# Kernel tuning notes

Measured on AMD Instinct MI355X. Metric: run time of the kernel, lower is better.

Reference implementation:

```python
import jax, jax.numpy as jnp
import numpy as np

N_NODES = 100000
N_EDGES = 6400000


def setup_inputs() -> dict:
    key = jax.random.key(0)
    k_x, k_e, k_w1, k_w2 = jax.random.split(key, 4)
    x = jax.random.normal(k_x, (N_NODES, 1), dtype=jnp.float32)
    edge_index = jax.random.randint(k_e, (2, N_EDGES), 0, N_NODES, dtype=jnp.int64)
    # Glorot-ish init for the tiny GCN linears
    W1 = jax.random.normal(k_w1, (1, 16), dtype=jnp.float32) * (1.0 / np.sqrt(1))
    b1 = jnp.zeros((16,), dtype=jnp.float32)
    W2 = jax.random.normal(k_w2, (16, 1), dtype=jnp.float32) * (1.0 / np.sqrt(16))
    b2 = jnp.zeros((1,), dtype=jnp.float32)
    return {"x": x, "edge_index": edge_index, "W1": W1, "b1": b1, "W2": W2, "b2": b2}


def _gcn_forward(x, row, col, norm, W1, b1, W2, b2, n):
    def conv(h, W, b):
        h = h @ W                                   # [N, d_out] linear first (PyG GCNConv)
        msg = h[row] * norm[:, None]                # gather + symmetric norm
        out = jax.ops.segment_sum(msg, col, num_segments=n)  # scatter-add to targets
        return out + b

    h = jax.nn.relu(conv(x, W1, b1))
    return conv(h, W2, b2)


def reference(x, edge_index, W1, b1, W2, b2):
    n = x.shape[0]
    # add self loops (GCNConv default add_self_loops=True)
    loop = jnp.arange(n, dtype=edge_index.dtype)
    row = jnp.concatenate([edge_index[0], loop])    # source j
    col = jnp.concatenate([edge_index[1], loop])    # target i
    # symmetric normalization D^{-1/2} (A+I) D^{-1/2}
    deg = jax.ops.segment_sum(jnp.ones_like(row, dtype=x.dtype), col, num_segments=n)
    deg_inv_sqrt = jnp.where(deg > 0, jax.lax.rsqrt(jnp.maximum(deg, 1.0)), 0.0)
    norm = deg_inv_sqrt[row] * deg_inv_sqrt[col]    # [E+N]
    return _gcn_forward(x, row, col, norm, W1, b1, W2, b2, n)
```

## Files before the change

kernel.cpp:

```cpp
#include <hip/hip_runtime.h>

#define BLK    256
#define NH     1024
#define SCAN_T 1024
#define SHIFT  13
#define CHUNK  8192
#define BPB    64
#define MAXNB  32



__global__ void k_hist(const int* __restrict__ col, int* __restrict__ hist,
                       int E, int NB) {
    __shared__ int h[MAXNB];
    for (int j = threadIdx.x; j < NB; j += BLK) h[j] = 0;
    __syncthreads();
    int stride = gridDim.x * blockDim.x;
    for (int e = blockIdx.x * blockDim.x + threadIdx.x; e < E; e += stride)
        atomicAdd(&h[col[e] >> SHIFT], 1);
    __syncthreads();
    for (int j = threadIdx.x; j < NB; j += BLK)
        hist[blockIdx.x * NB + j] = h[j];
}

__global__ void k_colscan(const int* __restrict__ hist, int* __restrict__ colOff,
                          int* __restrict__ totals, int NB) {
    __shared__ int lds[SCAN_T];
    int p = blockIdx.x, t = threadIdx.x;
    int v = hist[t * NB + p];
    lds[t] = v;
    __syncthreads();
    for (int off = 1; off < SCAN_T; off <<= 1) {
        int add = (t >= off) ? lds[t - off] : 0;
        __syncthreads();
        lds[t] += add;
        __syncthreads();
    }
    colOff[t * NB + p] = lds[t] - v;
    if (t == SCAN_T - 1) totals[p] = lds[t];
}

__global__ void k_binscan(const int* __restrict__ totals, int* __restrict__ binstart,
                          int NB) {
    if (blockIdx.x == 0 && threadIdx.x == 0) {
        int run = 0;
        for (int p = 0; p < NB; ++p) { binstart[p] = run; run += totals[p]; }
        binstart[NB] = run;
    }
}

__global__ void k_scatter(const int* __restrict__ row, const int* __restrict__ col,
                          const int* __restrict__ colOff, const int* __restrict__ binstart,
                          int* __restrict__ rows, int* __restrict__ colsl,
                          int E, int NB) {
    __shared__ int cur[MAXNB];
    for (int j = threadIdx.x; j < NB; j += BLK)
        cur[j] = binstart[j] + colOff[blockIdx.x * NB + j];
    __syncthreads();
    int stride = gridDim.x * blockDim.x;
    for (int e = blockIdx.x * blockDim.x + threadIdx.x; e < E; e += stride) {
        int c = col[e];
        int p = c >> SHIFT;
        int pos = atomicAdd(&cur[p], 1);
        rows[pos]  = row[e];
        colsl[pos] = c & (CHUNK - 1);
    }
}

template <bool GATHER>
__global__ void k_bagg(const int* __restrict__ rows, const int* __restrict__ colsl,
                       const int* __restrict__ binstart, const float* __restrict__ src,
                       float* __restrict__ partial) {
    __shared__ float acc[CHUNK];
    int p = blockIdx.x / BPB, q = blockIdx.x % BPB;
    for (int j = threadIdx.x; j < CHUNK; j += BLK) acc[j] = 0.0f;
    __syncthreads();
    int s = binstart[p], t = binstart[p + 1];
    long long len = t - s;
    int lo = s + (int)(len * q / BPB);
    int hi = s + (int)(len * (q + 1) / BPB);
    for (int e = lo + threadIdx.x; e < hi; e += BLK) {
        float v = GATHER ? src[rows[e]] : 1.0f;
        atomicAdd(&acc[colsl[e]], v);
    }
    __syncthreads();
    float* out = partial + (size_t)blockIdx.x * CHUNK;
    for (int j = threadIdx.x; j < CHUNK; j += BLK) out[j] = acc[j];
}

__device__ __forceinline__ float red_sum(const float* __restrict__ partial, int i) {
    int p = i >> SHIFT, il = i & (CHUNK - 1);
    const float* base = partial + ((size_t)p * BPB) * CHUNK + il;
    float s = 0.0f;
#pragma unroll
    for (int q = 0; q < BPB; ++q) s += base[(size_t)q * CHUNK];
    return s;
}

__global__ void k_red_deg_node1(const float* __restrict__ partial, const float* __restrict__ x,
                                float* __restrict__ dis, float* __restrict__ xs,
                                float* __restrict__ tself, int n) {
    int i = blockIdx.x * blockDim.x + threadIdx.x;
    if (i >= n) return;
    float d = rsqrtf(red_sum(partial, i) + 1.0f);
    dis[i] = d;
    float v = x[i] * d;
    xs[i] = v;
    tself[i] = v;
}

__global__ void k_red_node2(const float* __restrict__ partial, const float* __restrict__ dis,
                            float* __restrict__ t_gs, float* __restrict__ u,
                            const float* __restrict__ W1, const float* __restrict__ b1,
                            const float* __restrict__ W2, int n) {
    int i = blockIdx.x * blockDim.x + threadIdx.x;
    if (i >= n) return;
    float tt = t_gs[i] + red_sum(partial, i);
    float a = dis[i] * tt;
    float g = 0.0f;
#pragma unroll
    for (int k = 0; k < 16; ++k) {
        float h = fmaf(a, W1[k], b1[k]);
        h = fmaxf(h, 0.0f);
        g = fmaf(h, W2[k], g);
    }
    float v = g * dis[i];
    t_gs[i] = v;
    u[i]    = v;
}

__global__ void k_red_out(const float* __restrict__ partial, const float* __restrict__ dis,
                          float* __restrict__ u_out, const float* __restrict__ b2, int n) {
    int i = blockIdx.x * blockDim.x + threadIdx.x;
    if (i >= n) return;
    float uu = u_out[i] + red_sum(partial, i);
    u_out[i] = fmaf(dis[i], uu, b2[0]);
}


__global__ void k_zero(int* __restrict__ p, int n) {
    int i = blockIdx.x * blockDim.x + threadIdx.x;
    if (i < n) p[i] = 0;
}
__global__ void k_deg(const int* __restrict__ col, int* __restrict__ deg, int E) {
    int stride = gridDim.x * blockDim.x;
    for (int e = blockIdx.x * blockDim.x + threadIdx.x; e < E; e += stride)
        atomicAdd(&deg[col[e]], 1);
}
__global__ void k_agg(const int* __restrict__ row, const int* __restrict__ col,
                      const float* __restrict__ src, float* __restrict__ dst, int E) {
    int stride = gridDim.x * blockDim.x;
    for (int e = blockIdx.x * blockDim.x + threadIdx.x; e < E; e += stride)
        unsafeAtomicAdd(&dst[col[e]], src[row[e]]);
}
__global__ void k_node1(const float* __restrict__ x, int* __restrict__ deg_i,
                        float* __restrict__ xs, float* __restrict__ t, int n) {
    int i = blockIdx.x * blockDim.x + threadIdx.x;
    if (i < n) {
        float d = rsqrtf((float)deg_i[i] + 1.0f);
        reinterpret_cast<float*>(deg_i)[i] = d;
        float v = x[i] * d;
        xs[i] = v;
        t[i]  = v;
    }
}
__global__ void k_node2(const float* __restrict__ dis, float* __restrict__ t_gs,
                        const float* __restrict__ W1, const float* __restrict__ b1,
                        const float* __restrict__ W2, float* __restrict__ u, int n) {
    int i = blockIdx.x * blockDim.x + threadIdx.x;
    if (i < n) {
        float a = dis[i] * t_gs[i];
        float g = 0.0f;
#pragma unroll
        for (int k = 0; k < 16; ++k) {
            float h = fmaf(a, W1[k], b1[k]);
            h = fmaxf(h, 0.0f);
            g = fmaf(h, W2[k], g);
        }
        float v = g * dis[i];
        t_gs[i] = v;
        u[i]    = v;
    }
}
__global__ void k_out(const float* __restrict__ dis, float* __restrict__ u_out,
                      const float* __restrict__ b2, int n) {
    int i = blockIdx.x * blockDim.x + threadIdx.x;
    if (i < n) u_out[i] = fmaf(dis[i], u_out[i], b2[0]);
}


extern "C" void kernel_launch(void* const* d_in, const int* in_sizes, int n_in,
                              void* d_out, int out_size, void* d_ws, size_t ws_size,
                              hipStream_t stream) {
    const float* x   = (const float*)d_in[0];
    const int*   idx = (const int*)d_in[1];
    const float* W1  = (const float*)d_in[2];
    const float* b1  = (const float*)d_in[3];
    const float* W2  = (const float*)d_in[4];
    const float* b2  = (const float*)d_in[5];

    int n = in_sizes[0];
    int E = in_sizes[1] / 2;
    const int* row = idx;
    const int* col = idx + E;

    int NB = (n + CHUNK - 1) >> SHIFT;

    float* wsf = (float*)d_ws;
    size_t o = 0;
    float* dis      = wsf + o;            o += (size_t)n;
    float* ws1      = wsf + o;            o += (size_t)n;
    int*   hist     = (int*)(wsf + o);    o += (size_t)NH * NB;
    int*   colOff   = (int*)(wsf + o);    o += (size_t)NH * NB;
    int*   totals   = (int*)(wsf + o);    o += (size_t)NB;
    int*   binstart = (int*)(wsf + o);    o += (size_t)NB + 1;
    int*   rows     = (int*)(wsf + o);    o += (size_t)E;
    int*   colsl    = (int*)(wsf + o);    o += (size_t)E;
    float* partial  = wsf + o;            o += (size_t)NB * BPB * CHUNK;
    bool can_bin = (NB <= MAXNB) && (ws_size >= o * 4 + 64);

    float* out = (float*)d_out;
    int nb = (n + BLK - 1) / BLK;

    if (can_bin) {
        k_hist   <<<NH, BLK,    0, stream>>>(col, hist, E, NB);
        k_colscan<<<NB, SCAN_T, 0, stream>>>(hist, colOff, totals, NB);
        k_binscan<<<1,  64,     0, stream>>>(totals, binstart, NB);
        k_scatter<<<NH, BLK,    0, stream>>>(row, col, colOff, binstart, rows, colsl, E, NB);
        k_bagg<false><<<NB * BPB, BLK, 0, stream>>>(rows, colsl, binstart, nullptr, partial);
        k_red_deg_node1<<<nb, BLK, 0, stream>>>(partial, x, dis, out, ws1, n);
        k_bagg<true> <<<NB * BPB, BLK, 0, stream>>>(rows, colsl, binstart, out, partial);
        k_red_node2  <<<nb, BLK, 0, stream>>>(partial, dis, ws1, out, W1, b1, W2, n);
        k_bagg<true> <<<NB * BPB, BLK, 0, stream>>>(rows, colsl, binstart, ws1, partial);
        k_red_out    <<<nb, BLK, 0, stream>>>(partial, dis, out, b2, n);
    } else {
        int*   ws0i = (int*)d_ws;
        float* ws0f = (float*)d_ws;
        int eb = ((E + 3) / 4 + BLK - 1) / BLK;
        if (eb > 2048) eb = 2048;
        k_zero <<<nb, BLK, 0, stream>>>(ws0i, n);
        k_deg  <<<eb, BLK, 0, stream>>>(col, ws0i, E);
        k_node1<<<nb, BLK, 0, stream>>>(x, ws0i, out, ws1, n);
        k_agg  <<<eb, BLK, 0, stream>>>(row, col, out, ws1, E);
        k_node2<<<nb, BLK, 0, stream>>>(ws0f, ws1, W1, b1, W2, out, n);
        k_agg  <<<eb, BLK, 0, stream>>>(row, col, ws1, out, E);
        k_out  <<<nb, BLK, 0, stream>>>(ws0f, out, b2, n);
    }
}
```

Measured before the change: 302.5 us.

## Shrink bin chunks and pack source/target into one int per edge

Node bins shrink from 8192 to 512 nodes, and per-bin block splitting drops from 64 to 8. This makes the per-block partial-sum buffer, and its reduction reads, much smaller and uses far less LDS per block. The scatter step now writes a single packed word (source index shifted left, plus local target) instead of two separate arrays, halving edge-list traffic for all three aggregation passes. The trade-offs are more bins, so scatter writes are spread over more destinations, and a guard that requires node counts below 2^22 so the packing fits. The fallback path gets a no-op ternary on its launch size.

```diff
diff --git a/kernel.cpp b/kernel.cpp
--- a/kernel.cpp
+++ b/kernel.cpp
@@ -3,10 +3,10 @@
 #define BLK    256
 #define NH     1024
 #define SCAN_T 1024
-#define SHIFT  13
-#define CHUNK  8192
-#define BPB    64
-#define MAXNB  32
+#define SHIFT  9
+#define CHUNK  512
+#define BPB    8
+#define MAXNB  256
 
 
 
@@ -51,8 +51,7 @@
 
 __global__ void k_scatter(const int* __restrict__ row, const int* __restrict__ col,
                           const int* __restrict__ colOff, const int* __restrict__ binstart,
-                          int* __restrict__ rows, int* __restrict__ colsl,
-                          int E, int NB) {
+                          int* __restrict__ pk, int E, int NB) {
     __shared__ int cur[MAXNB];
     for (int j = threadIdx.x; j < NB; j += BLK)
         cur[j] = binstart[j] + colOff[blockIdx.x * NB + j];
@@ -62,15 +61,13 @@
         int c = col[e];
         int p = c >> SHIFT;
         int pos = atomicAdd(&cur[p], 1);
-        rows[pos]  = row[e];
-        colsl[pos] = c & (CHUNK - 1);
+        pk[pos] = (row[e] << SHIFT) | (c & (CHUNK - 1));
     }
 }
 
 template <bool GATHER>
-__global__ void k_bagg(const int* __restrict__ rows, const int* __restrict__ colsl,
-                       const int* __restrict__ binstart, const float* __restrict__ src,
-                       float* __restrict__ partial) {
+__global__ void k_bagg(const int* __restrict__ pk, const int* __restrict__ binstart,
+                       const float* __restrict__ src, float* __restrict__ partial) {
     __shared__ float acc[CHUNK];
     int p = blockIdx.x / BPB, q = blockIdx.x % BPB;
     for (int j = threadIdx.x; j < CHUNK; j += BLK) acc[j] = 0.0f;
@@ -80,8 +77,9 @@
     int lo = s + (int)(len * q / BPB);
     int hi = s + (int)(len * (q + 1) / BPB);
     for (int e = lo + threadIdx.x; e < hi; e += BLK) {
-        float v = GATHER ? src[rows[e]] : 1.0f;
-        atomicAdd(&acc[colsl[e]], v);
+        int v = pk[e];
+        float val = GATHER ? src[((unsigned)v) >> SHIFT] : 1.0f;
+        atomicAdd(&acc[v & (CHUNK - 1)], val);
     }
     __syncthreads();
     float* out = partial + (size_t)blockIdx.x * CHUNK;
@@ -214,10 +212,10 @@
     int*   colOff   = (int*)(wsf + o);    o += (size_t)NH * NB;
     int*   totals   = (int*)(wsf + o);    o += (size_t)NB;
     int*   binstart = (int*)(wsf + o);    o += (size_t)NB + 1;
-    int*   rows     = (int*)(wsf + o);    o += (size_t)E;
-    int*   colsl    = (int*)(wsf + o);    o += (size_t)E;
+    int*   pk       = (int*)(wsf + o);    o += (size_t)E;
     float* partial  = wsf + o;            o += (size_t)NB * BPB * CHUNK;
-    bool can_bin = (NB <= MAXNB) && (ws_size >= o * 4 + 64);
+    bool can_bin = (NB <= MAXNB) && (ws_size >= o * 4 + 64) &&
+                   (n < (1 << (31 - SHIFT)));
 
     float* out = (float*)d_out;
     int nb = (n + BLK - 1) / BLK;
@@ -226,12 +224,12 @@
         k_hist   <<<NH, BLK,    0, stream>>>(col, hist, E, NB);
         k_colscan<<<NB, SCAN_T, 0, stream>>>(hist, colOff, totals, NB);
         k_binscan<<<1,  64,     0, stream>>>(totals, binstart, NB);
-        k_scatter<<<NH, BLK,    0, stream>>>(row, col, colOff, binstart, rows, colsl, E, NB);
-        k_bagg<false><<<NB * BPB, BLK, 0, stream>>>(rows, colsl, binstart, nullptr, partial);
+        k_scatter<<<NH, BLK,    0, stream>>>(row, col, colOff, binstart, pk, E, NB);
+        k_bagg<false><<<NB * BPB, BLK, 0, stream>>>(pk, binstart, nullptr, partial);
         k_red_deg_node1<<<nb, BLK, 0, stream>>>(partial, x, dis, out, ws1, n);
-        k_bagg<true> <<<NB * BPB, BLK, 0, stream>>>(rows, colsl, binstart, out, partial);
+        k_bagg<true> <<<NB * BPB, BLK, 0, stream>>>(pk, binstart, out, partial);
         k_red_node2  <<<nb, BLK, 0, stream>>>(partial, dis, ws1, out, W1, b1, W2, n);
-        k_bagg<true> <<<NB * BPB, BLK, 0, stream>>>(rows, colsl, binstart, ws1, partial);
+        k_bagg<true> <<<NB * BPB, BLK, 0, stream>>>(pk, binstart, ws1, partial);
         k_red_out    <<<nb, BLK, 0, stream>>>(partial, dis, out, b2, n);
     } else {
         int*   ws0i = (int*)d_ws;
@@ -242,7 +240,7 @@
         k_deg  <<<eb, BLK, 0, stream>>>(col, ws0i, E);
         k_node1<<<nb, BLK, 0, stream>>>(x, ws0i, out, ws1, n);
         k_agg  <<<eb, BLK, 0, stream>>>(row, col, out, ws1, E);
-        k_node2<<<nb, BLK, 0, stream>>>(ws0f, ws1, W1, b1, W2, out, n);
+        k_node2<<<ws_size ? nb : nb, BLK, 0, stream>>>(ws0f, ws1, W1, b1, W2, out, n);
         k_agg  <<<eb, BLK, 0, stream>>>(row, col, ws1, out, E);
         k_out  <<<nb, BLK, 0, stream>>>(ws0f, out, b2, n);
     }
```

After: 297.6 us. Within noise of the previous version (-1.6%).
